# Optimization experiments

Hardware: AMD Instinct MI355X
Metric: run time of the kernel (lower is better)

Reference implementation:

```python
import jax, jax.numpy as jnp
import numpy as np

B, N, F_IN, F_OUT = 8, 8192, 128, 128
E = 1_048_576
BN = B * N


def setup_inputs() -> dict:
    key = jax.random.key(0)
    ks = jax.random.split(key, 9)
    glorot = (6.0 / (F_IN + F_OUT)) ** 0.5
    return {
        "X": jax.random.normal(ks[0], (B, N, F_IN), dtype=jnp.float32),
        "W0": jax.random.uniform(ks[1], (F_IN, F_OUT), jnp.float32, -glorot, glorot),
        "W1": jax.random.uniform(ks[2], (F_IN, F_OUT), jnp.float32, -glorot, glorot),
        "rows0": jax.random.randint(ks[3], (E,), 0, BN, dtype=jnp.int32),
        "cols0": jax.random.randint(ks[4], (E,), 0, BN, dtype=jnp.int32),
        "vals0": jax.random.uniform(ks[5], (E,), dtype=jnp.float32),
        "rows1": jax.random.randint(ks[6], (E,), 0, BN, dtype=jnp.int32),
        "cols1": jax.random.randint(ks[7], (E,), 0, BN, dtype=jnp.int32),
        "vals1": jax.random.uniform(ks[8], (E,), dtype=jnp.float32),
    }


def _spmm(rows, cols, vals, H, n):
    # COO sparse [n, n] @ dense H [n, F]: gather source rows, scale, scatter-add.
    return jax.ops.segment_sum(vals[:, None] * H[cols], rows, num_segments=n)


def reference(X, W0, W1, rows0, cols0, vals0, rows1, cols1, vals1):
    b, n, f_in = X.shape
    X2 = X.reshape(-1, f_in)                      # [B*N, F_in]
    h0 = _spmm(rows0, cols0, vals0, X2 @ W0, b * n)  # filter_0 @ (X W0)
    h1 = _spmm(rows1, cols1, vals1, X2 @ W1, b * n)  # filter_1 @ (X W1)
    out = jax.nn.relu(h0 + h1).reshape(b, n, -1)  # add_n + relu
    return out
```

## Files before the change

kernel.cpp:

```cpp
#include <hip/hip_runtime.h>


typedef unsigned int   uint;
typedef unsigned short ushort;
typedef unsigned char  uchar;
typedef float f32x4 __attribute__((ext_vector_type(4)));
typedef int   i32x4 __attribute__((ext_vector_type(4)));

constexpr int NB  = 256;
constexpr int EPB = 8192;

__device__ __forceinline__ ushort f2bf(float f) {
    uint u = __float_as_uint(f);
    u += 0x7fffu + ((u >> 16) & 1u);
    return (ushort)(u >> 16);
}
__device__ __forceinline__ float bf2f(ushort h) {
    return __uint_as_float((uint)h << 16);
}

#define ACC_FENCE(a) asm volatile("s_nop 7\n\ts_nop 7" : "+v"(a))

__global__ __launch_bounds__(64) void w_swz(const float* __restrict__ W0,
                                            const float* __restrict__ W1,
                                            uint4* __restrict__ Wswz) {
    const int bx = blockIdx.x;
    const int f  = bx >> 5;
    const int ct = (bx >> 2) & 7;
    const int kt = bx & 3;
    const int l  = threadIdx.x;
    const float* W = f ? W1 : W0;
    const int kbase = kt * 32 + (l >> 4) * 8;
    const int col   = ct * 16 + (l & 15);
    ushort h[8];
#pragma unroll
    for (int j = 0; j < 8; ++j)
        h[j] = f2bf(W[(kbase + j) * 128 + col]);
    uint4 o;
    o.x = (uint)h[0] | ((uint)h[1] << 16);
    o.y = (uint)h[2] | ((uint)h[3] << 16);
    o.z = (uint)h[4] | ((uint)h[5] << 16);
    o.w = (uint)h[6] | ((uint)h[7] << 16);
    Wswz[((f * 8 + ct) * 4 + kt) * 64 + l] = o;
}

__global__ __launch_bounds__(256) void gemm_mfma(const float* __restrict__ X,
                                                 const i32x4* __restrict__ Wswz,
                                                 ushort* __restrict__ H, int BN) {
    __shared__ ushort xs_hi[64][136];
    __shared__ ushort xs_lo[64][136];
    const int tid = threadIdx.x;
    const int l = tid & 63;
    const int w = tid >> 6;
    const long rbase = (long)blockIdx.x * 64;

    const float4* Xv = reinterpret_cast<const float4*>(X + rbase * 128);
#pragma unroll
    for (int i = 0; i < 8; ++i) {
        int idx = i * 256 + tid;
        int row = idx >> 5, c4 = idx & 31;
        float4 v = Xv[idx];
        ushort4 hi, lo;
        hi.x = f2bf(v.x); lo.x = f2bf(v.x - bf2f(hi.x));
        hi.y = f2bf(v.y); lo.y = f2bf(v.y - bf2f(hi.y));
        hi.z = f2bf(v.z); lo.z = f2bf(v.z - bf2f(hi.z));
        hi.w = f2bf(v.w); lo.w = f2bf(v.w - bf2f(hi.w));
        *reinterpret_cast<ushort4*>(&xs_hi[row][c4 * 4]) = hi;
        *reinterpret_cast<ushort4*>(&xs_lo[row][c4 * 4]) = lo;
    }
    __syncthreads();

    i32x4 a_hi[4], a_lo[4];
    const int arow = w * 16 + (l & 15);
    const int kb = (l >> 4) * 8;
#pragma unroll
    for (int kt = 0; kt < 4; ++kt) {
        a_hi[kt] = *reinterpret_cast<const i32x4*>(&xs_hi[arow][kt * 32 + kb]);
        a_lo[kt] = *reinterpret_cast<const i32x4*>(&xs_lo[arow][kt * 32 + kb]);
    }

    f32x4 acc[2][8];
#pragma unroll
    for (int f = 0; f < 2; ++f)
#pragma unroll
        for (int ct = 0; ct < 8; ++ct)
            acc[f][ct] = (f32x4)0.0f;

#pragma unroll
    for (int ct = 0; ct < 8; ++ct)
#pragma unroll
        for (int f = 0; f < 2; ++f)
#pragma unroll
            for (int kt = 0; kt < 4; ++kt) {
                i32x4 b = Wswz[((f * 8 + ct) * 4 + kt) * 64 + l];
                asm volatile("v_mfma_f32_16x16x32_bf16 %0, %1, %2, %0"
                             : "+v"(acc[f][ct]) : "v"(a_hi[kt]), "v"(b));
                asm volatile("v_mfma_f32_16x16x32_bf16 %0, %1, %2, %0"
                             : "+v"(acc[f][ct]) : "v"(a_lo[kt]), "v"(b));
            }

#pragma unroll
    for (int ct = 0; ct < 8; ++ct)
#pragma unroll
        for (int f = 0; f < 2; ++f) {
            f32x4 a = acc[f][ct];
            ACC_FENCE(a);
            ushort* Hf = H + (size_t)f * BN * 128;
            size_t base = (size_t)(rbase + w * 16 + (l >> 4) * 4) * 128
                        + ct * 16 + (l & 15);
            Hf[base]       = f2bf(a.x);
            Hf[base + 128] = f2bf(a.y);
            Hf[base + 256] = f2bf(a.z);
            Hf[base + 384] = f2bf(a.w);
        }
}

__global__ __launch_bounds__(256) void hist_coarse(const int* __restrict__ r0,
                                                   const int* __restrict__ r1,
                                                   int* __restrict__ cnt, int E) {
    __shared__ int h[NB];
    const int f = blockIdx.y, t = threadIdx.x;
    const int* rows = f ? r1 : r0;
    h[t] = 0;
    __syncthreads();
    const int base = blockIdx.x * EPB;
    for (int k = 0; k < EPB / 256; ++k) {
        int e = base + k * 256 + t;
        if (e < E) atomicAdd(&h[rows[e] >> 8], 1);
    }
    __syncthreads();
    if (h[t]) atomicAdd(&cnt[f * NB + t], h[t]);
}

__global__ __launch_bounds__(256) void scan_coarse(const int* __restrict__ cnt,
                                                   int* __restrict__ bbase,
                                                   int* __restrict__ bcur,
                                                   int* __restrict__ row_ptr,
                                                   int rp_stride, int BN, int E) {
    __shared__ int s[NB];
    const int f = blockIdx.x, t = threadIdx.x;
    int v = cnt[f * NB + t];
    s[t] = v;
    __syncthreads();
    for (int off = 1; off < NB; off <<= 1) {
        int u = (t >= off) ? s[t - off] : 0;
        __syncthreads();
        s[t] += u;
        __syncthreads();
    }
    int base = s[t] - v;
    bbase[f * NB + t] = base;
    bcur [f * NB + t] = base;
    if (t == NB - 1) row_ptr[(size_t)f * rp_stride + BN] = E;
}

__global__ __launch_bounds__(256) void partition(const int* __restrict__ r0,
                                                 const int* __restrict__ c0,
                                                 const float* __restrict__ v0,
                                                 const int* __restrict__ r1,
                                                 const int* __restrict__ c1,
                                                 const float* __restrict__ v1,
                                                 int* __restrict__ bcur,
                                                 uint* __restrict__ cvy,
                                                 uchar* __restrict__ cvr, int E) {
    __shared__ int h[NB];
    __shared__ int cur[NB];
    const int f = blockIdx.y, t = threadIdx.x;
    const int*   rows = f ? r1 : r0;
    const int*   cols = f ? c1 : c0;
    const float* vals = f ? v1 : v0;
    const int base = blockIdx.x * EPB;

    h[t] = 0;
    __syncthreads();
    for (int k = 0; k < EPB / 256; ++k) {
        int e = base + k * 256 + t;
        if (e < E) atomicAdd(&h[rows[e] >> 8], 1);
    }
    __syncthreads();
    cur[t] = atomicAdd(&bcur[f * NB + t], h[t]);
    __syncthreads();

    uint*  yout = cvy + (size_t)f * E;
    uchar* rout = cvr + (size_t)f * E;
    for (int k = 0; k < EPB / 256; ++k) {
        int e = base + k * 256 + t;
        if (e < E) {
            int r = rows[e];
            int pos = atomicAdd(&cur[r >> 8], 1);
            yout[pos] = ((uint)cols[e] << 16) | (uint)f2bf(vals[e]);
            rout[pos] = (uchar)(r & 255);
        }
    }
}

__global__ __launch_bounds__(256) void bucket_sort(const uint* __restrict__ cvy,
                                                   const uchar* __restrict__ cvr,
                                                   const int* __restrict__ bbase,
                                                   const int* __restrict__ bcur,
                                                   uint* __restrict__ cv,
                                                   int* __restrict__ row_ptr,
                                                   int rp_stride, int E) {
    __shared__ int h[NB];
    __shared__ int s[NB];
    __shared__ int curs[NB];
    const int f = blockIdx.y, b = blockIdx.x, t = threadIdx.x;
    const int start = bbase[f * NB + b];
    const int end   = bcur [f * NB + b];
    const uint*  yin = cvy + (size_t)f * E;
    const uchar* rin = cvr + (size_t)f * E;

    h[t] = 0;
    __syncthreads();
    for (int i = start + t; i < end; i += 256)
        atomicAdd(&h[rin[i]], 1);
    __syncthreads();

    int v = h[t];
    s[t] = v;
    __syncthreads();
    for (int off = 1; off < NB; off <<= 1) {
        int u = (t >= off) ? s[t - off] : 0;
        __syncthreads();
        s[t] += u;
        __syncthreads();
    }
    int rowbase = start + s[t] - v;
    row_ptr[(size_t)f * rp_stride + b * 256 + t] = rowbase;
    curs[t] = rowbase;
    __syncthreads();

    uint* outp = cv + (size_t)f * E;
    for (int i = start + t; i < end; i += 256) {
        int pos = atomicAdd(&curs[rin[i]], 1);
        outp[pos] = yin[i];
    }
}

__global__ __launch_bounds__(256) void hist2(const int* __restrict__ r0,
                                             const int* __restrict__ r1,
                                             int* __restrict__ cnt, int E, int BN) {
    int e = blockIdx.x * 256 + threadIdx.x;
    const int* rows = blockIdx.y ? r1 : r0;
    if (e < E) atomicAdd(&cnt[(size_t)blockIdx.y * BN + rows[e]], 1);
}

__global__ __launch_bounds__(256) void scan2(int* __restrict__ cnt,
                                             int* __restrict__ row_ptr,
                                             int n, int rp_stride) {
    __shared__ int ssum[256];
    int* counts = cnt + (size_t)blockIdx.x * n;
    int* rp     = row_ptr + (size_t)blockIdx.x * rp_stride;
    const int t = threadIdx.x;
    const int chunk = n / 256;
    const int base = t * chunk;
    const int4* c4 = reinterpret_cast<const int4*>(counts + base);
    int s = 0;
#pragma unroll 4
    for (int i = 0; i < chunk / 4; ++i) {
        int4 v = c4[i];
        s += v.x + v.y + v.z + v.w;
    }
    ssum[t] = s;
    __syncthreads();
    for (int off = 1; off < 256; off <<= 1) {
        int u = (t >= off) ? ssum[t - off] : 0;
        __syncthreads();
        ssum[t] += u;
        __syncthreads();
    }
    int run = ssum[t] - s;
    int4* rp4 = reinterpret_cast<int4*>(rp + base);
    int4* cu4 = reinterpret_cast<int4*>(counts + base);
#pragma unroll 4
    for (int i = 0; i < chunk / 4; ++i) {
        int4 v = c4[i];
        int4 p;
        p.x = run; run += v.x;
        p.y = run; run += v.y;
        p.z = run; run += v.z;
        p.w = run; run += v.w;
        rp4[i] = p;
        cu4[i] = p;
    }
    if (t == 255) rp[n] = run;
}

__global__ __launch_bounds__(256) void permute2(const int* __restrict__ r0,
                                                const int* __restrict__ c0,
                                                const float* __restrict__ v0,
                                                const int* __restrict__ r1,
                                                const int* __restrict__ c1,
                                                const float* __restrict__ v1,
                                                int* __restrict__ cursor,
                                                uint* __restrict__ cv, int E, int BN) {
    int f = blockIdx.y;
    const int*   rows = f ? r1 : r0;
    const int*   cols = f ? c1 : c0;
    const float* vals = f ? v1 : v0;
    int e = blockIdx.x * 256 + threadIdx.x;
    if (e < E) {
        int r = rows[e];
        int pos = atomicAdd(&cursor[(size_t)f * BN + r], 1);
        cv[(size_t)f * E + pos] = ((uint)cols[e] << 16) | (uint)f2bf(vals[e]);
    }
}

__device__ __forceinline__ void fma4(float4& a, float v, ushort4 h) {
    a.x = fmaf(v, bf2f(h.x), a.x);
    a.y = fmaf(v, bf2f(h.y), a.y);
    a.z = fmaf(v, bf2f(h.z), a.z);
    a.w = fmaf(v, bf2f(h.w), a.w);
}

__global__ __launch_bounds__(256) void gather_fused(const int* __restrict__ row_ptr,
                                                    int rp_stride,
                                                    const uint* __restrict__ cv, int E,
                                                    const ushort* __restrict__ H, int BN,
                                                    float* __restrict__ out) {
    const int half = threadIdx.x >> 5;
    const int sub  = threadIdx.x & 31;
    const int r = blockIdx.x * 8 + half;

    float4 a0 = make_float4(0.f, 0.f, 0.f, 0.f);
    float4 a1 = make_float4(0.f, 0.f, 0.f, 0.f);
    float4 a2 = make_float4(0.f, 0.f, 0.f, 0.f);
    float4 a3 = make_float4(0.f, 0.f, 0.f, 0.f);

#pragma unroll
    for (int f = 0; f < 2; ++f) {
        const int*    rp  = row_ptr + (size_t)f * rp_stride;
        const uint*   cvf = cv + (size_t)f * E;
        const ushort* Hf  = H + (size_t)f * BN * 128;
        int e = rp[r];
        const int t = rp[r + 1];
        for (; e + 7 < t; e += 8) {
            uint p0 = cvf[e],     p1 = cvf[e + 1], p2 = cvf[e + 2], p3 = cvf[e + 3];
            uint p4 = cvf[e + 4], p5 = cvf[e + 5], p6 = cvf[e + 6], p7 = cvf[e + 7];
            ushort4 h0 = reinterpret_cast<const ushort4*>(Hf + (size_t)(p0 >> 16) * 128)[sub];
            ushort4 h1 = reinterpret_cast<const ushort4*>(Hf + (size_t)(p1 >> 16) * 128)[sub];
            ushort4 h2 = reinterpret_cast<const ushort4*>(Hf + (size_t)(p2 >> 16) * 128)[sub];
            ushort4 h3 = reinterpret_cast<const ushort4*>(Hf + (size_t)(p3 >> 16) * 128)[sub];
            ushort4 h4 = reinterpret_cast<const ushort4*>(Hf + (size_t)(p4 >> 16) * 128)[sub];
            ushort4 h5 = reinterpret_cast<const ushort4*>(Hf + (size_t)(p5 >> 16) * 128)[sub];
            ushort4 h6 = reinterpret_cast<const ushort4*>(Hf + (size_t)(p6 >> 16) * 128)[sub];
            ushort4 h7 = reinterpret_cast<const ushort4*>(Hf + (size_t)(p7 >> 16) * 128)[sub];
            fma4(a0, __uint_as_float(p0 << 16), h0);
            fma4(a1, __uint_as_float(p1 << 16), h1);
            fma4(a2, __uint_as_float(p2 << 16), h2);
            fma4(a3, __uint_as_float(p3 << 16), h3);
            fma4(a0, __uint_as_float(p4 << 16), h4);
            fma4(a1, __uint_as_float(p5 << 16), h5);
            fma4(a2, __uint_as_float(p6 << 16), h6);
            fma4(a3, __uint_as_float(p7 << 16), h7);
        }
        for (; e + 3 < t; e += 4) {
            uint p0 = cvf[e], p1 = cvf[e + 1], p2 = cvf[e + 2], p3 = cvf[e + 3];
            ushort4 h0 = reinterpret_cast<const ushort4*>(Hf + (size_t)(p0 >> 16) * 128)[sub];
            ushort4 h1 = reinterpret_cast<const ushort4*>(Hf + (size_t)(p1 >> 16) * 128)[sub];
            ushort4 h2 = reinterpret_cast<const ushort4*>(Hf + (size_t)(p2 >> 16) * 128)[sub];
            ushort4 h3 = reinterpret_cast<const ushort4*>(Hf + (size_t)(p3 >> 16) * 128)[sub];
            fma4(a0, __uint_as_float(p0 << 16), h0);
            fma4(a1, __uint_as_float(p1 << 16), h1);
            fma4(a2, __uint_as_float(p2 << 16), h2);
            fma4(a3, __uint_as_float(p3 << 16), h3);
        }
        for (; e < t; ++e) {
            uint p0 = cvf[e];
            ushort4 h0 = reinterpret_cast<const ushort4*>(Hf + (size_t)(p0 >> 16) * 128)[sub];
            fma4(a0, __uint_as_float(p0 << 16), h0);
        }
    }

    float4 o;
    o.x = fmaxf((a0.x + a1.x) + (a2.x + a3.x), 0.0f);
    o.y = fmaxf((a0.y + a1.y) + (a2.y + a3.y), 0.0f);
    o.z = fmaxf((a0.z + a1.z) + (a2.z + a3.z), 0.0f);
    o.w = fmaxf((a0.w + a1.w) + (a2.w + a3.w), 0.0f);
    reinterpret_cast<float4*>(out)[(size_t)r * 32 + sub] = o;
}

extern "C" void kernel_launch(void* const* d_in, const int* in_sizes, int n_in,
                              void* d_out, int out_size, void* d_ws, size_t ws_size,
                              hipStream_t stream) {
    const float* X     = (const float*)d_in[0];
    const float* W0    = (const float*)d_in[1];
    const float* W1    = (const float*)d_in[2];
    const int*   rows0 = (const int*)d_in[3];
    const int*   cols0 = (const int*)d_in[4];
    const float* vals0 = (const float*)d_in[5];
    const int*   rows1 = (const int*)d_in[6];
    const int*   cols1 = (const int*)d_in[7];
    const float* vals1 = (const float*)d_in[8];
    float* out = (float*)d_out;

    const int BN = in_sizes[0] / 128;
    const int E  = in_sizes[3];
    const int rp_stride = BN + 16;

    char* ws = (char*)d_ws;
    size_t off = 0;
    auto alloc = [&](size_t bytes) {
        void* p = ws + off;
        off = (off + bytes + 255) & ~(size_t)255;
        return p;
    };
    ushort* H       = (ushort*)alloc((size_t)2 * BN * 128 * sizeof(ushort));
    uint*   cv      = (uint*)  alloc((size_t)2 * E * sizeof(uint));
    int*    row_ptr = (int*)   alloc((size_t)2 * rp_stride * sizeof(int));
    uint4*  Wswz    = (uint4*) alloc((size_t)2 * 128 * 128 * sizeof(ushort));

    const size_t need_big = off + (size_t)2 * E * sizeof(uint)
                                + (size_t)2 * E * sizeof(uchar)
                                + 3 * (size_t)2 * NB * sizeof(int) + 1024;

    const int gath_blocks = BN / 8;

    w_swz<<<64, 64, 0, stream>>>(W0, W1, Wswz);
    gemm_mfma<<<BN / 64, 256, 0, stream>>>(X, (const i32x4*)Wswz, H, BN);

    if (ws_size >= need_big && BN == 65536) {
        uint*  cvy   = (uint*) alloc((size_t)2 * E * sizeof(uint));
        uchar* cvr   = (uchar*)alloc((size_t)2 * E * sizeof(uchar));
        int*   cnt   = (int*)  alloc((size_t)2 * NB * sizeof(int));
        int*   bbase = (int*)  alloc((size_t)2 * NB * sizeof(int));
        int*   bcur  = (int*)  alloc((size_t)2 * NB * sizeof(int));

        const int part_blocks = (E + EPB - 1) / EPB;
        hipMemsetAsync(cnt, 0, (size_t)2 * NB * sizeof(int), stream);
        hist_coarse<<<dim3(part_blocks, 2), 256, 0, stream>>>(rows0, rows1, cnt, E);
        scan_coarse<<<2, 256, 0, stream>>>(cnt, bbase, bcur, row_ptr, rp_stride, BN, E);
        partition<<<dim3(part_blocks, 2), 256, 0, stream>>>(rows0, cols0, vals0,
                                                            rows1, cols1, vals1,
                                                            bcur, cvy, cvr, E);
        bucket_sort<<<dim3(NB, 2), 256, 0, stream>>>(cvy, cvr, bbase, bcur,
                                                     cv, row_ptr, rp_stride, E);
    } else {
        int* cursor = (int*)alloc((size_t)2 * BN * sizeof(int));
        const int edge_blocks = (E + 255) / 256;
        hipMemsetAsync(cursor, 0, (size_t)2 * BN * sizeof(int), stream);
        hist2<<<dim3(edge_blocks, 2), 256, 0, stream>>>(rows0, rows1, cursor, E, BN);
        scan2<<<2, 256, 0, stream>>>(cursor, row_ptr, BN, rp_stride);
        permute2<<<dim3(edge_blocks, 2), 256, 0, stream>>>(rows0, cols0, vals0,
                                                           rows1, cols1, vals1,
                                                           cursor, cv, E, BN);
    }

    gather_fused<<<gath_blocks, 256, 0, stream>>>(row_ptr, rp_stride, cv, E, H, BN, out);
}
```

Before: 179.1 us.

## Fuse column-bucket partition with GEMM and make row sort stable by column

```diff
diff --git a/kernel.cpp b/kernel.cpp
--- a/kernel.cpp
+++ b/kernel.cpp
@@ -44,15 +44,113 @@
     Wswz[((f * 8 + ct) * 4 + kt) * 64 + l] = o;
 }
 
-__global__ __launch_bounds__(256) void gemm_mfma(const float* __restrict__ X,
-                                                 const i32x4* __restrict__ Wswz,
-                                                 ushort* __restrict__ H, int BN) {
+__global__ __launch_bounds__(256) void hist_both(const int* __restrict__ r0,
+                                                 const int* __restrict__ c0,
+                                                 const int* __restrict__ r1,
+                                                 const int* __restrict__ c1,
+                                                 int* __restrict__ cnt_col,
+                                                 int* __restrict__ cnt_row, int E) {
+    __shared__ int hc[NB], hr[NB];
+    const int f = blockIdx.y, t = threadIdx.x;
+    const int* rows = f ? r1 : r0;
+    const int* cols = f ? c1 : c0;
+    hc[t] = 0; hr[t] = 0;
+    __syncthreads();
+    const int base = blockIdx.x * EPB;
+    for (int k = 0; k < EPB / 256; ++k) {
+        int e = base + k * 256 + t;
+        if (e < E) {
+            atomicAdd(&hc[cols[e] >> 8], 1);
+            atomicAdd(&hr[rows[e] >> 8], 1);
+        }
+    }
+    __syncthreads();
+    if (hc[t]) atomicAdd(&cnt_col[f * NB + t], hc[t]);
+    if (hr[t]) atomicAdd(&cnt_row[f * NB + t], hr[t]);
+}
+
+__global__ __launch_bounds__(256) void scan_both(const int* __restrict__ cnt_col,
+                                                 const int* __restrict__ cnt_row,
+                                                 int* __restrict__ ccur,
+                                                 int* __restrict__ bbase,
+                                                 int* __restrict__ bcur,
+                                                 int* __restrict__ row_ptr,
+                                                 int rp_stride, int BN, int E) {
+    __shared__ int s[NB];
+    const int bx = blockIdx.x, t = threadIdx.x;
+    const int kind = bx >> 1, f = bx & 1;
+    const int* cnt = kind ? cnt_row : cnt_col;
+    int v = cnt[f * NB + t];
+    s[t] = v;
+    __syncthreads();
+    for (int off = 1; off < NB; off <<= 1) {
+        int u = (t >= off) ? s[t - off] : 0;
+        __syncthreads();
+        s[t] += u;
+        __syncthreads();
+    }
+    int base = s[t] - v;
+    if (kind == 0) {
+        ccur[f * NB + t] = base;
+    } else {
+        bbase[f * NB + t] = base;
+        bcur [f * NB + t] = base;
+        if (t == NB - 1) row_ptr[(size_t)f * rp_stride + BN] = E;
+    }
+}
+
+__global__ __launch_bounds__(256) void fused_p0_gemm(
+        const float* __restrict__ X, const i32x4* __restrict__ Wswz,
+        ushort* __restrict__ H, int BN,
+        const int* __restrict__ r0, const int* __restrict__ c0,
+        const float* __restrict__ v0,
+        const int* __restrict__ r1, const int* __restrict__ c1,
+        const float* __restrict__ v1,
+        int* __restrict__ ccur, uint* __restrict__ colv,
+        ushort* __restrict__ crow, int E, int partb) {
     __shared__ ushort xs_hi[64][136];
     __shared__ ushort xs_lo[64][136];
+    __shared__ int ph[NB], pcur[NB];
+
+    const int bx  = blockIdx.x;
     const int tid = threadIdx.x;
+
+    if (bx < 2 * partb) {
+        const int f  = bx / partb;
+        const int px = bx % partb;
+        const int*   rows = f ? r1 : r0;
+        const int*   cols = f ? c1 : c0;
+        const float* vals = f ? v1 : v0;
+        const int base = px * EPB;
+
+        ph[tid] = 0;
+        __syncthreads();
+        for (int k = 0; k < EPB / 256; ++k) {
+            int e = base + k * 256 + tid;
+            if (e < E) atomicAdd(&ph[cols[e] >> 8], 1);
+        }
+        __syncthreads();
+        pcur[tid] = atomicAdd(&ccur[f * NB + tid], ph[tid]);
+        __syncthreads();
+
+        uint*   yo = colv + (size_t)f * E;
+        ushort* ro = crow + (size_t)f * E;
+        for (int k = 0; k < EPB / 256; ++k) {
+            int e = base + k * 256 + tid;
+            if (e < E) {
+                int c = cols[e];
+                int pos = atomicAdd(&pcur[c >> 8], 1);
+                yo[pos] = ((uint)c << 16) | (uint)f2bf(vals[e]);
+                ro[pos] = (ushort)rows[e];
+            }
+        }
+        return;
+    }
+
+    const int gx = bx - 2 * partb;
     const int l = tid & 63;
     const int w = tid >> 6;
-    const long rbase = (long)blockIdx.x * 64;
+    const long rbase = (long)gx * 64;
 
     const float4* Xv = reinterpret_cast<const float4*>(X + rbase * 128);
 #pragma unroll
@@ -113,6 +211,83 @@
             Hf[base + 256] = f2bf(a.z);
             Hf[base + 384] = f2bf(a.w);
         }
+}
+
+__global__ __launch_bounds__(256) void partition_row2(const uint* __restrict__ colv,
+                                                      const ushort* __restrict__ crow,
+                                                      int* __restrict__ bcur,
+                                                      uint* __restrict__ cvy,
+                                                      uchar* __restrict__ cvr, int E) {
+    __shared__ int h[NB], cur[NB];
+    const int f = blockIdx.y, t = threadIdx.x;
+    const uint*   cvl = colv + (size_t)f * E;
+    const ushort* cr  = crow + (size_t)f * E;
+    const int base = blockIdx.x * EPB;
+
+    h[t] = 0;
+    __syncthreads();
+    for (int k = 0; k < EPB / 256; ++k) {
+        int e = base + k * 256 + t;
+        if (e < E) atomicAdd(&h[cr[e] >> 8], 1);
+    }
+    __syncthreads();
+    cur[t] = atomicAdd(&bcur[f * NB + t], h[t]);
+    __syncthreads();
+
+    uint*  yo = cvy + (size_t)f * E;
+    uchar* ro = cvr + (size_t)f * E;
+    for (int k = 0; k < EPB / 256; ++k) {
+        int e = base + k * 256 + t;
+        if (e < E) {
+            ushort r = cr[e];
+            int pos = atomicAdd(&cur[r >> 8], 1);
+            yo[pos] = cvl[e];
+            ro[pos] = (uchar)(r & 255);
+        }
+    }
+}
+
+__global__ __launch_bounds__(256) void bucket_sort(const uint* __restrict__ cvy,
+                                                   const uchar* __restrict__ cvr,
+                                                   const int* __restrict__ bbase,
+                                                   const int* __restrict__ bcur,
+                                                   uint* __restrict__ cv,
+                                                   int* __restrict__ row_ptr,
+                                                   int rp_stride, int E) {
+    __shared__ int h[NB];
+    __shared__ int s[NB];
+    __shared__ int curs[NB];
+    const int f = blockIdx.y, b = blockIdx.x, t = threadIdx.x;
+    const int start = bbase[f * NB + b];
+    const int end   = bcur [f * NB + b];
+    const uint*  yin = cvy + (size_t)f * E;
+    const uchar* rin = cvr + (size_t)f * E;
+
+    h[t] = 0;
+    __syncthreads();
+    for (int i = start + t; i < end; i += 256)
+        atomicAdd(&h[rin[i]], 1);
+    __syncthreads();
+
+    int v = h[t];
+    s[t] = v;
+    __syncthreads();
+    for (int off = 1; off < NB; off <<= 1) {
+        int u = (t >= off) ? s[t - off] : 0;
+        __syncthreads();
+        s[t] += u;
+        __syncthreads();
+    }
+    int rowbase = start + s[t] - v;
+    row_ptr[(size_t)f * rp_stride + b * 256 + t] = rowbase;
+    curs[t] = rowbase;
+    __syncthreads();
+
+    uint* outp = cv + (size_t)f * E;
+    for (int i = start + t; i < end; i += 256) {
+        int pos = atomicAdd(&curs[rin[i]], 1);
+        outp[pos] = yin[i];
+    }
 }
 
 __global__ __launch_bounds__(256) void hist_coarse(const int* __restrict__ r0,
@@ -194,47 +369,75 @@
     }
 }
 
-__global__ __launch_bounds__(256) void bucket_sort(const uint* __restrict__ cvy,
-                                                   const uchar* __restrict__ cvr,
-                                                   const int* __restrict__ bbase,
-                                                   const int* __restrict__ bcur,
-                                                   uint* __restrict__ cv,
-                                                   int* __restrict__ row_ptr,
-                                                   int rp_stride, int E) {
-    __shared__ int h[NB];
-    __shared__ int s[NB];
-    __shared__ int curs[NB];
-    const int f = blockIdx.y, b = blockIdx.x, t = threadIdx.x;
-    const int start = bbase[f * NB + b];
-    const int end   = bcur [f * NB + b];
-    const uint*  yin = cvy + (size_t)f * E;
-    const uchar* rin = cvr + (size_t)f * E;
-
-    h[t] = 0;
-    __syncthreads();
-    for (int i = start + t; i < end; i += 256)
-        atomicAdd(&h[rin[i]], 1);
-    __syncthreads();
-
-    int v = h[t];
-    s[t] = v;
-    __syncthreads();
-    for (int off = 1; off < NB; off <<= 1) {
-        int u = (t >= off) ? s[t - off] : 0;
-        __syncthreads();
-        s[t] += u;
-        __syncthreads();
-    }
-    int rowbase = start + s[t] - v;
-    row_ptr[(size_t)f * rp_stride + b * 256 + t] = rowbase;
-    curs[t] = rowbase;
-    __syncthreads();
-
-    uint* outp = cv + (size_t)f * E;
-    for (int i = start + t; i < end; i += 256) {
-        int pos = atomicAdd(&curs[rin[i]], 1);
-        outp[pos] = yin[i];
-    }
+__global__ __launch_bounds__(256) void gemm_mfma(const float* __restrict__ X,
+                                                 const i32x4* __restrict__ Wswz,
+                                                 ushort* __restrict__ H, int BN) {
+    __shared__ ushort xs_hi[64][136];
+    __shared__ ushort xs_lo[64][136];
+    const int tid = threadIdx.x;
+    const int l = tid & 63;
+    const int w = tid >> 6;
+    const long rbase = (long)blockIdx.x * 64;
+
+    const float4* Xv = reinterpret_cast<const float4*>(X + rbase * 128);
+#pragma unroll
+    for (int i = 0; i < 8; ++i) {
+        int idx = i * 256 + tid;
+        int row = idx >> 5, c4 = idx & 31;
+        float4 v = Xv[idx];
+        ushort4 hi, lo;
+        hi.x = f2bf(v.x); lo.x = f2bf(v.x - bf2f(hi.x));
+        hi.y = f2bf(v.y); lo.y = f2bf(v.y - bf2f(hi.y));
+        hi.z = f2bf(v.z); lo.z = f2bf(v.z - bf2f(hi.z));
+        hi.w = f2bf(v.w); lo.w = f2bf(v.w - bf2f(hi.w));
+        *reinterpret_cast<ushort4*>(&xs_hi[row][c4 * 4]) = hi;
+        *reinterpret_cast<ushort4*>(&xs_lo[row][c4 * 4]) = lo;
+    }
+    __syncthreads();
+
+    i32x4 a_hi[4], a_lo[4];
+    const int arow = w * 16 + (l & 15);
+    const int kb = (l >> 4) * 8;
+#pragma unroll
+    for (int kt = 0; kt < 4; ++kt) {
+        a_hi[kt] = *reinterpret_cast<const i32x4*>(&xs_hi[arow][kt * 32 + kb]);
+        a_lo[kt] = *reinterpret_cast<const i32x4*>(&xs_lo[arow][kt * 32 + kb]);
+    }
+
+    f32x4 acc[2][8];
+#pragma unroll
+    for (int f = 0; f < 2; ++f)
+#pragma unroll
+        for (int ct = 0; ct < 8; ++ct)
+            acc[f][ct] = (f32x4)0.0f;
+
+#pragma unroll
+    for (int ct = 0; ct < 8; ++ct)
+#pragma unroll
+        for (int f = 0; f < 2; ++f)
+#pragma unroll
+            for (int kt = 0; kt < 4; ++kt) {
+                i32x4 b = Wswz[((f * 8 + ct) * 4 + kt) * 64 + l];
+                asm volatile("v_mfma_f32_16x16x32_bf16 %0, %1, %2, %0"
+                             : "+v"(acc[f][ct]) : "v"(a_hi[kt]), "v"(b));
+                asm volatile("v_mfma_f32_16x16x32_bf16 %0, %1, %2, %0"
+                             : "+v"(acc[f][ct]) : "v"(a_lo[kt]), "v"(b));
+            }
+
+#pragma unroll
+    for (int ct = 0; ct < 8; ++ct)
+#pragma unroll
+        for (int f = 0; f < 2; ++f) {
+            f32x4 a = acc[f][ct];
+            ACC_FENCE(a);
+            ushort* Hf = H + (size_t)f * BN * 128;
+            size_t base = (size_t)(rbase + w * 16 + (l >> 4) * 4) * 128
+                        + ct * 16 + (l & 15);
+            Hf[base]       = f2bf(a.x);
+            Hf[base + 128] = f2bf(a.y);
+            Hf[base + 256] = f2bf(a.z);
+            Hf[base + 384] = f2bf(a.w);
+        }
 }
 
 __global__ __launch_bounds__(256) void hist2(const int* __restrict__ r0,
@@ -397,6 +600,8 @@
     const int BN = in_sizes[0] / 128;
     const int E  = in_sizes[3];
     const int rp_stride = BN + 16;
+    const int partb = (E + EPB - 1) / EPB;
+    const int gath_blocks = BN / 8;
 
     char* ws = (char*)d_ws;
     size_t off = 0;
@@ -406,34 +611,66 @@
         return p;
     };
     ushort* H       = (ushort*)alloc((size_t)2 * BN * 128 * sizeof(ushort));
-    uint*   cv      = (uint*)  alloc((size_t)2 * E * sizeof(uint));
     int*    row_ptr = (int*)   alloc((size_t)2 * rp_stride * sizeof(int));
     uint4*  Wswz    = (uint4*) alloc((size_t)2 * 128 * 128 * sizeof(ushort));
-
-    const size_t need_big = off + (size_t)2 * E * sizeof(uint)
-                                + (size_t)2 * E * sizeof(uchar)
-                                + 3 * (size_t)2 * NB * sizeof(int) + 1024;
-
-    const int gath_blocks = BN / 8;
+    const size_t common = off;
+
+    uint*   colv = (uint*)  alloc((size_t)2 * E * sizeof(uint));
+    ushort* crow = (ushort*)alloc((size_t)2 * E * sizeof(ushort));
+    uint*   cvy  = (uint*)  alloc((size_t)2 * E * sizeof(uint));
+    uchar*  cvr  = (uchar*) alloc((size_t)2 * E * sizeof(uchar));
+    int*    cnts = (int*)   alloc((size_t)4 * NB * sizeof(int));
+    int*    ccur = (int*)   alloc((size_t)2 * NB * sizeof(int));
+    int*    bbase= (int*)   alloc((size_t)2 * NB * sizeof(int));
+    int*    bcur = (int*)   alloc((size_t)2 * NB * sizeof(int));
+    const size_t need_new = off;
+    uint* cv_new = colv;
 
     w_swz<<<64, 64, 0, stream>>>(W0, W1, Wswz);
+
+    if (ws_size >= need_new && BN == 65536) {
+        int* cnt_col = cnts;
+        int* cnt_row = cnts + 2 * NB;
+        hipMemsetAsync(cnts, 0, (size_t)4 * NB * sizeof(int), stream);
+        hist_both<<<dim3(partb, 2), 256, 0, stream>>>(rows0, cols0, rows1, cols1,
+                                                      cnt_col, cnt_row, E);
+        scan_both<<<4, 256, 0, stream>>>(cnt_col, cnt_row, ccur, bbase, bcur,
+                                         row_ptr, rp_stride, BN, E);
+        fused_p0_gemm<<<2 * partb + BN / 64, 256, 0, stream>>>(
+            X, (const i32x4*)Wswz, H, BN,
+            rows0, cols0, vals0, rows1, cols1, vals1,
+            ccur, colv, crow, E, partb);
+        partition_row2<<<dim3(partb, 2), 256, 0, stream>>>(colv, crow, bcur,
+                                                           cvy, cvr, E);
+        bucket_sort<<<dim3(NB, 2), 256, 0, stream>>>(cvy, cvr, bbase, bcur,
+                                                     cv_new, row_ptr, rp_stride, E);
+        gather_fused<<<gath_blocks, 256, 0, stream>>>(row_ptr, rp_stride, cv_new,
+                                                      E, H, BN, out);
+        return;
+    }
+
+    off = common;
+    uint* cv = (uint*)alloc((size_t)2 * E * sizeof(uint));
+    const size_t need_r7 = off + (size_t)2 * E * sizeof(uint)
+                               + (size_t)2 * E * sizeof(uchar)
+                               + 3 * (size_t)2 * NB * sizeof(int) + 1024;
+
     gemm_mfma<<<BN / 64, 256, 0, stream>>>(X, (const i32x4*)Wswz, H, BN);
 
-    if (ws_size >= need_big && BN == 65536) {
-        uint*  cvy   = (uint*) alloc((size_t)2 * E * sizeof(uint));
-        uchar* cvr   = (uchar*)alloc((size_t)2 * E * sizeof(uchar));
+    if (ws_size >= need_r7 && BN == 65536) {
+        uint*  cvy2  = (uint*) alloc((size_t)2 * E * sizeof(uint));
+        uchar* cvr2  = (uchar*)alloc((size_t)2 * E * sizeof(uchar));
         int*   cnt   = (int*)  alloc((size_t)2 * NB * sizeof(int));
-        int*   bbase = (int*)  alloc((size_t)2 * NB * sizeof(int));
-        int*   bcur  = (int*)  alloc((size_t)2 * NB * sizeof(int));
-
-        const int part_blocks = (E + EPB - 1) / EPB;
+        int*   bb2   = (int*)  alloc((size_t)2 * NB * sizeof(int));
+        int*   bc2   = (int*)  alloc((size_t)2 * NB * sizeof(int));
+
         hipMemsetAsync(cnt, 0, (size_t)2 * NB * sizeof(int), stream);
-        hist_coarse<<<dim3(part_blocks, 2), 256, 0, stream>>>(rows0, rows1, cnt, E);
-        scan_coarse<<<2, 256, 0, stream>>>(cnt, bbase, bcur, row_ptr, rp_stride, BN, E);
-        partition<<<dim3(part_blocks, 2), 256, 0, stream>>>(rows0, cols0, vals0,
-                                                            rows1, cols1, vals1,
-                                                            bcur, cvy, cvr, E);
-        bucket_sort<<<dim3(NB, 2), 256, 0, stream>>>(cvy, cvr, bbase, bcur,
+        hist_coarse<<<dim3(partb, 2), 256, 0, stream>>>(rows0, rows1, cnt, E);
+        scan_coarse<<<2, 256, 0, stream>>>(cnt, bb2, bc2, row_ptr, rp_stride, BN, E);
+        partition<<<dim3(partb, 2), 256, 0, stream>>>(rows0, cols0, vals0,
+                                                      rows1, cols1, vals1,
+                                                      bc2, cvy2, cvr2, E);
+        bucket_sort<<<dim3(NB, 2), 256, 0, stream>>>(cvy2, cvr2, bb2, bc2,
                                                      cv, row_ptr, rp_stride, E);
     } else {
         int* cursor = (int*)alloc((size_t)2 * BN * sizeof(int));
```

Measured after the change: 218.6 us. +22.0%, slower.

## Fuse per-bucket row sort into the SpMM gather kernel using LDS

Applied to the files above, without the earlier changes.

```diff
diff --git a/kernel.cpp b/kernel.cpp
--- a/kernel.cpp
+++ b/kernel.cpp
@@ -9,6 +9,7 @@
 
 constexpr int NB  = 256;
 constexpr int EPB = 8192;
+constexpr int CAP = 8192;
 
 __device__ __forceinline__ ushort f2bf(float f) {
     uint u = __float_as_uint(f);
@@ -134,9 +135,7 @@
 
 __global__ __launch_bounds__(256) void scan_coarse(const int* __restrict__ cnt,
                                                    int* __restrict__ bbase,
-                                                   int* __restrict__ bcur,
-                                                   int* __restrict__ row_ptr,
-                                                   int rp_stride, int BN, int E) {
+                                                   int* __restrict__ bcur) {
     __shared__ int s[NB];
     const int f = blockIdx.x, t = threadIdx.x;
     int v = cnt[f * NB + t];
@@ -151,7 +150,6 @@
     int base = s[t] - v;
     bbase[f * NB + t] = base;
     bcur [f * NB + t] = base;
-    if (t == NB - 1) row_ptr[(size_t)f * rp_stride + BN] = E;
 }
 
 __global__ __launch_bounds__(256) void partition(const int* __restrict__ r0,
@@ -194,118 +192,6 @@
     }
 }
 
-__global__ __launch_bounds__(256) void bucket_sort(const uint* __restrict__ cvy,
-                                                   const uchar* __restrict__ cvr,
-                                                   const int* __restrict__ bbase,
-                                                   const int* __restrict__ bcur,
-                                                   uint* __restrict__ cv,
-                                                   int* __restrict__ row_ptr,
-                                                   int rp_stride, int E) {
-    __shared__ int h[NB];
-    __shared__ int s[NB];
-    __shared__ int curs[NB];
-    const int f = blockIdx.y, b = blockIdx.x, t = threadIdx.x;
-    const int start = bbase[f * NB + b];
-    const int end   = bcur [f * NB + b];
-    const uint*  yin = cvy + (size_t)f * E;
-    const uchar* rin = cvr + (size_t)f * E;
-
-    h[t] = 0;
-    __syncthreads();
-    for (int i = start + t; i < end; i += 256)
-        atomicAdd(&h[rin[i]], 1);
-    __syncthreads();
-
-    int v = h[t];
-    s[t] = v;
-    __syncthreads();
-    for (int off = 1; off < NB; off <<= 1) {
-        int u = (t >= off) ? s[t - off] : 0;
-        __syncthreads();
-        s[t] += u;
-        __syncthreads();
-    }
-    int rowbase = start + s[t] - v;
-    row_ptr[(size_t)f * rp_stride + b * 256 + t] = rowbase;
-    curs[t] = rowbase;
-    __syncthreads();
-
-    uint* outp = cv + (size_t)f * E;
-    for (int i = start + t; i < end; i += 256) {
-        int pos = atomicAdd(&curs[rin[i]], 1);
-        outp[pos] = yin[i];
-    }
-}
-
-__global__ __launch_bounds__(256) void hist2(const int* __restrict__ r0,
-                                             const int* __restrict__ r1,
-                                             int* __restrict__ cnt, int E, int BN) {
-    int e = blockIdx.x * 256 + threadIdx.x;
-    const int* rows = blockIdx.y ? r1 : r0;
-    if (e < E) atomicAdd(&cnt[(size_t)blockIdx.y * BN + rows[e]], 1);
-}
-
-__global__ __launch_bounds__(256) void scan2(int* __restrict__ cnt,
-                                             int* __restrict__ row_ptr,
-                                             int n, int rp_stride) {
-    __shared__ int ssum[256];
-    int* counts = cnt + (size_t)blockIdx.x * n;
-    int* rp     = row_ptr + (size_t)blockIdx.x * rp_stride;
-    const int t = threadIdx.x;
-    const int chunk = n / 256;
-    const int base = t * chunk;
-    const int4* c4 = reinterpret_cast<const int4*>(counts + base);
-    int s = 0;
-#pragma unroll 4
-    for (int i = 0; i < chunk / 4; ++i) {
-        int4 v = c4[i];
-        s += v.x + v.y + v.z + v.w;
-    }
-    ssum[t] = s;
-    __syncthreads();
-    for (int off = 1; off < 256; off <<= 1) {
-        int u = (t >= off) ? ssum[t - off] : 0;
-        __syncthreads();
-        ssum[t] += u;
-        __syncthreads();
-    }
-    int run = ssum[t] - s;
-    int4* rp4 = reinterpret_cast<int4*>(rp + base);
-    int4* cu4 = reinterpret_cast<int4*>(counts + base);
-#pragma unroll 4
-    for (int i = 0; i < chunk / 4; ++i) {
-        int4 v = c4[i];
-        int4 p;
-        p.x = run; run += v.x;
-        p.y = run; run += v.y;
-        p.z = run; run += v.z;
-        p.w = run; run += v.w;
-        rp4[i] = p;
-        cu4[i] = p;
-    }
-    if (t == 255) rp[n] = run;
-}
-
-__global__ __launch_bounds__(256) void permute2(const int* __restrict__ r0,
-                                                const int* __restrict__ c0,
-                                                const float* __restrict__ v0,
-                                                const int* __restrict__ r1,
-                                                const int* __restrict__ c1,
-                                                const float* __restrict__ v1,
-                                                int* __restrict__ cursor,
-                                                uint* __restrict__ cv, int E, int BN) {
-    int f = blockIdx.y;
-    const int*   rows = f ? r1 : r0;
-    const int*   cols = f ? c1 : c0;
-    const float* vals = f ? v1 : v0;
-    int e = blockIdx.x * 256 + threadIdx.x;
-    if (e < E) {
-        int r = rows[e];
-        int pos = atomicAdd(&cursor[(size_t)f * BN + r], 1);
-        cv[(size_t)f * E + pos] = ((uint)cols[e] << 16) | (uint)f2bf(vals[e]);
-    }
-}
-
 __device__ __forceinline__ void fma4(float4& a, float v, ushort4 h) {
     a.x = fmaf(v, bf2f(h.x), a.x);
     a.y = fmaf(v, bf2f(h.y), a.y);
@@ -313,71 +199,144 @@
     a.w = fmaf(v, bf2f(h.w), a.w);
 }
 
-__global__ __launch_bounds__(256) void gather_fused(const int* __restrict__ row_ptr,
-                                                    int rp_stride,
-                                                    const uint* __restrict__ cv, int E,
-                                                    const ushort* __restrict__ H, int BN,
-                                                    float* __restrict__ out) {
-    const int half = threadIdx.x >> 5;
-    const int sub  = threadIdx.x & 31;
-    const int r = blockIdx.x * 8 + half;
-
-    float4 a0 = make_float4(0.f, 0.f, 0.f, 0.f);
-    float4 a1 = make_float4(0.f, 0.f, 0.f, 0.f);
-    float4 a2 = make_float4(0.f, 0.f, 0.f, 0.f);
-    float4 a3 = make_float4(0.f, 0.f, 0.f, 0.f);
-
-#pragma unroll
+__global__ __launch_bounds__(1024) void sort_gather(
+        const uint* __restrict__ cvy, const uchar* __restrict__ cvr,
+        const int* __restrict__ bbase, const int* __restrict__ bcur,
+        const ushort* __restrict__ H, int BN,
+        float* __restrict__ out, int E) {
+    __shared__ uint cvl[2][CAP];
+    __shared__ int rp[2][NB + 1];
+    __shared__ int hcnt[NB];
+    __shared__ int curs[NB];
+    __shared__ int sstart[2], scount[2], sovf[2];
+
+    const int b = blockIdx.x;
+    const int t = threadIdx.x;
+
+#pragma unroll 1
     for (int f = 0; f < 2; ++f) {
-        const int*    rp  = row_ptr + (size_t)f * rp_stride;
-        const uint*   cvf = cv + (size_t)f * E;
-        const ushort* Hf  = H + (size_t)f * BN * 128;
-        int e = rp[r];
-        const int t = rp[r + 1];
-        for (; e + 7 < t; e += 8) {
-            uint p0 = cvf[e],     p1 = cvf[e + 1], p2 = cvf[e + 2], p3 = cvf[e + 3];
-            uint p4 = cvf[e + 4], p5 = cvf[e + 5], p6 = cvf[e + 6], p7 = cvf[e + 7];
-            ushort4 h0 = reinterpret_cast<const ushort4*>(Hf + (size_t)(p0 >> 16) * 128)[sub];
-            ushort4 h1 = reinterpret_cast<const ushort4*>(Hf + (size_t)(p1 >> 16) * 128)[sub];
-            ushort4 h2 = reinterpret_cast<const ushort4*>(Hf + (size_t)(p2 >> 16) * 128)[sub];
-            ushort4 h3 = reinterpret_cast<const ushort4*>(Hf + (size_t)(p3 >> 16) * 128)[sub];
-            ushort4 h4 = reinterpret_cast<const ushort4*>(Hf + (size_t)(p4 >> 16) * 128)[sub];
-            ushort4 h5 = reinterpret_cast<const ushort4*>(Hf + (size_t)(p5 >> 16) * 128)[sub];
-            ushort4 h6 = reinterpret_cast<const ushort4*>(Hf + (size_t)(p6 >> 16) * 128)[sub];
-            ushort4 h7 = reinterpret_cast<const ushort4*>(Hf + (size_t)(p7 >> 16) * 128)[sub];
-            fma4(a0, __uint_as_float(p0 << 16), h0);
-            fma4(a1, __uint_as_float(p1 << 16), h1);
-            fma4(a2, __uint_as_float(p2 << 16), h2);
-            fma4(a3, __uint_as_float(p3 << 16), h3);
-            fma4(a0, __uint_as_float(p4 << 16), h4);
-            fma4(a1, __uint_as_float(p5 << 16), h5);
-            fma4(a2, __uint_as_float(p6 << 16), h6);
-            fma4(a3, __uint_as_float(p7 << 16), h7);
-        }
-        for (; e + 3 < t; e += 4) {
-            uint p0 = cvf[e], p1 = cvf[e + 1], p2 = cvf[e + 2], p3 = cvf[e + 3];
-            ushort4 h0 = reinterpret_cast<const ushort4*>(Hf + (size_t)(p0 >> 16) * 128)[sub];
-            ushort4 h1 = reinterpret_cast<const ushort4*>(Hf + (size_t)(p1 >> 16) * 128)[sub];
-            ushort4 h2 = reinterpret_cast<const ushort4*>(Hf + (size_t)(p2 >> 16) * 128)[sub];
-            ushort4 h3 = reinterpret_cast<const ushort4*>(Hf + (size_t)(p3 >> 16) * 128)[sub];
-            fma4(a0, __uint_as_float(p0 << 16), h0);
-            fma4(a1, __uint_as_float(p1 << 16), h1);
-            fma4(a2, __uint_as_float(p2 << 16), h2);
-            fma4(a3, __uint_as_float(p3 << 16), h3);
-        }
-        for (; e < t; ++e) {
-            uint p0 = cvf[e];
-            ushort4 h0 = reinterpret_cast<const ushort4*>(Hf + (size_t)(p0 >> 16) * 128)[sub];
-            fma4(a0, __uint_as_float(p0 << 16), h0);
-        }
-    }
-
-    float4 o;
-    o.x = fmaxf((a0.x + a1.x) + (a2.x + a3.x), 0.0f);
-    o.y = fmaxf((a0.y + a1.y) + (a2.y + a3.y), 0.0f);
-    o.z = fmaxf((a0.z + a1.z) + (a2.z + a3.z), 0.0f);
-    o.w = fmaxf((a0.w + a1.w) + (a2.w + a3.w), 0.0f);
-    reinterpret_cast<float4*>(out)[(size_t)r * 32 + sub] = o;
+        if (t == 0) {
+            int s0 = bbase[f * NB + b];
+            int e0 = bcur [f * NB + b];
+            sstart[f] = s0;
+            scount[f] = e0 - s0;
+            sovf[f]   = (e0 - s0) > CAP;
+        }
+        if (t < NB) hcnt[t] = 0;
+        __syncthreads();
+        const int s = sstart[f], n = scount[f];
+        const uchar* rin = cvr + (size_t)f * E + s;
+        const uint*  yin = cvy + (size_t)f * E + s;
+        for (int i = t; i < n; i += 1024)
+            atomicAdd(&hcnt[rin[i]], 1);
+        __syncthreads();
+        int v = (t < NB) ? hcnt[t] : 0;
+        if (t < NB) curs[t] = v;
+        __syncthreads();
+        for (int off = 1; off < NB; off <<= 1) {
+            int u = 0;
+            if (t < NB && t >= off) u = curs[t - off];
+            __syncthreads();
+            if (t < NB) curs[t] += u;
+            __syncthreads();
+        }
+        if (t < NB) {
+            int ex = curs[t] - v;
+            rp[f][t] = ex;
+            curs[t] = ex;
+        }
+        if (t == 0) rp[f][NB] = n;
+        __syncthreads();
+        if (!sovf[f]) {
+            for (int i = t; i < n; i += 1024) {
+                uchar r = rin[i];
+                int pos = atomicAdd(&curs[r], 1);
+                cvl[f][pos] = __builtin_nontemporal_load(&yin[i]);
+            }
+        }
+        __syncthreads();
+    }
+
+    const int half = t >> 5;
+    const int sub  = t & 31;
+    f32x4* outv = reinterpret_cast<f32x4*>(out);
+
+#pragma unroll 1
+    for (int k = 0; k < 8; ++k) {
+        const int lr = k * 32 + half;
+        const long gr = (long)b * NB + lr;
+
+        float4 a0 = make_float4(0.f, 0.f, 0.f, 0.f);
+        float4 a1 = make_float4(0.f, 0.f, 0.f, 0.f);
+        float4 a2 = make_float4(0.f, 0.f, 0.f, 0.f);
+        float4 a3 = make_float4(0.f, 0.f, 0.f, 0.f);
+
+#pragma unroll
+        for (int f = 0; f < 2; ++f) {
+            const ushort* Hf = H + (size_t)f * BN * 128;
+            if (!sovf[f]) {
+                int e = rp[f][lr];
+                const int e1 = rp[f][lr + 1];
+                for (; e + 7 < e1; e += 8) {
+                    uint p0 = cvl[f][e],     p1 = cvl[f][e + 1];
+                    uint p2 = cvl[f][e + 2], p3 = cvl[f][e + 3];
+                    uint p4 = cvl[f][e + 4], p5 = cvl[f][e + 5];
+                    uint p6 = cvl[f][e + 6], p7 = cvl[f][e + 7];
+                    ushort4 h0 = reinterpret_cast<const ushort4*>(Hf + (size_t)(p0 >> 16) * 128)[sub];
+                    ushort4 h1 = reinterpret_cast<const ushort4*>(Hf + (size_t)(p1 >> 16) * 128)[sub];
+                    ushort4 h2 = reinterpret_cast<const ushort4*>(Hf + (size_t)(p2 >> 16) * 128)[sub];
+                    ushort4 h3 = reinterpret_cast<const ushort4*>(Hf + (size_t)(p3 >> 16) * 128)[sub];
+                    ushort4 h4 = reinterpret_cast<const ushort4*>(Hf + (size_t)(p4 >> 16) * 128)[sub];
+                    ushort4 h5 = reinterpret_cast<const ushort4*>(Hf + (size_t)(p5 >> 16) * 128)[sub];
+                    ushort4 h6 = reinterpret_cast<const ushort4*>(Hf + (size_t)(p6 >> 16) * 128)[sub];
+                    ushort4 h7 = reinterpret_cast<const ushort4*>(Hf + (size_t)(p7 >> 16) * 128)[sub];
+                    fma4(a0, __uint_as_float(p0 << 16), h0);
+                    fma4(a1, __uint_as_float(p1 << 16), h1);
+                    fma4(a2, __uint_as_float(p2 << 16), h2);
+                    fma4(a3, __uint_as_float(p3 << 16), h3);
+                    fma4(a0, __uint_as_float(p4 << 16), h4);
+                    fma4(a1, __uint_as_float(p5 << 16), h5);
+                    fma4(a2, __uint_as_float(p6 << 16), h6);
+                    fma4(a3, __uint_as_float(p7 << 16), h7);
+                }
+                for (; e + 3 < e1; e += 4) {
+                    uint p0 = cvl[f][e],     p1 = cvl[f][e + 1];
+                    uint p2 = cvl[f][e + 2], p3 = cvl[f][e + 3];
+                    ushort4 h0 = reinterpret_cast<const ushort4*>(Hf + (size_t)(p0 >> 16) * 128)[sub];
+                    ushort4 h1 = reinterpret_cast<const ushort4*>(Hf + (size_t)(p1 >> 16) * 128)[sub];
+                    ushort4 h2 = reinterpret_cast<const ushort4*>(Hf + (size_t)(p2 >> 16) * 128)[sub];
+                    ushort4 h3 = reinterpret_cast<const ushort4*>(Hf + (size_t)(p3 >> 16) * 128)[sub];
+                    fma4(a0, __uint_as_float(p0 << 16), h0);
+                    fma4(a1, __uint_as_float(p1 << 16), h1);
+                    fma4(a2, __uint_as_float(p2 << 16), h2);
+                    fma4(a3, __uint_as_float(p3 << 16), h3);
+                }
+                for (; e < e1; ++e) {
+                    uint p0 = cvl[f][e];
+                    ushort4 h0 = reinterpret_cast<const ushort4*>(Hf + (size_t)(p0 >> 16) * 128)[sub];
+                    fma4(a0, __uint_as_float(p0 << 16), h0);
+                }
+            } else {
+                const int s = sstart[f], n = scount[f];
+                const uchar* rin = cvr + (size_t)f * E + s;
+                const uint*  yin = cvy + (size_t)f * E + s;
+                for (int i = 0; i < n; ++i) {
+                    if (rin[i] == (uchar)lr) {
+                        uint p0 = yin[i];
+                        ushort4 h0 = reinterpret_cast<const ushort4*>(Hf + (size_t)(p0 >> 16) * 128)[sub];
+                        fma4(a0, __uint_as_float(p0 << 16), h0);
+                    }
+                }
+            }
+        }
+
+        f32x4 o;
+        o.x = fmaxf((a0.x + a1.x) + (a2.x + a3.x), 0.0f);
+        o.y = fmaxf((a0.y + a1.y) + (a2.y + a3.y), 0.0f);
+        o.z = fmaxf((a0.z + a1.z) + (a2.z + a3.z), 0.0f);
+        o.w = fmaxf((a0.w + a1.w) + (a2.w + a3.w), 0.0f);
+        __builtin_nontemporal_store(o, outv + gr * 32 + sub);
+    }
 }
 
 extern "C" void kernel_launch(void* const* d_in, const int* in_sizes, int n_in,
@@ -396,7 +355,7 @@
 
     const int BN = in_sizes[0] / 128;
     const int E  = in_sizes[3];
-    const int rp_stride = BN + 16;
+    const int partb = (E + EPB - 1) / EPB;
 
     char* ws = (char*)d_ws;
     size_t off = 0;
@@ -405,46 +364,22 @@
         off = (off + bytes + 255) & ~(size_t)255;
         return p;
     };
-    ushort* H       = (ushort*)alloc((size_t)2 * BN * 128 * sizeof(ushort));
-    uint*   cv      = (uint*)  alloc((size_t)2 * E * sizeof(uint));
-    int*    row_ptr = (int*)   alloc((size_t)2 * rp_stride * sizeof(int));
-    uint4*  Wswz    = (uint4*) alloc((size_t)2 * 128 * 128 * sizeof(ushort));
-
-    const size_t need_big = off + (size_t)2 * E * sizeof(uint)
-                                + (size_t)2 * E * sizeof(uchar)
-                                + 3 * (size_t)2 * NB * sizeof(int) + 1024;
-
-    const int gath_blocks = BN / 8;
+    ushort* H     = (ushort*)alloc((size_t)2 * BN * 128 * sizeof(ushort));
+    uint4*  Wswz  = (uint4*) alloc((size_t)2 * 128 * 128 * sizeof(ushort));
+    uint*   cvy   = (uint*)  alloc((size_t)2 * E * sizeof(uint));
+    uchar*  cvr   = (uchar*) alloc((size_t)2 * E * sizeof(uchar));
+    int*    cnt   = (int*)   alloc((size_t)2 * NB * sizeof(int));
+    int*    bbase = (int*)   alloc((size_t)2 * NB * sizeof(int));
+    int*    bcur  = (int*)   alloc((size_t)2 * NB * sizeof(int));
 
     w_swz<<<64, 64, 0, stream>>>(W0, W1, Wswz);
     gemm_mfma<<<BN / 64, 256, 0, stream>>>(X, (const i32x4*)Wswz, H, BN);
 
-    if (ws_size >= need_big && BN == 65536) {
-        uint*  cvy   = (uint*) alloc((size_t)2 * E * sizeof(uint));
-        uchar* cvr   = (uchar*)alloc((size_t)2 * E * sizeof(uchar));
-        int*   cnt   = (int*)  alloc((size_t)2 * NB * sizeof(int));
-        int*   bbase = (int*)  alloc((size_t)2 * NB * sizeof(int));
-        int*   bcur  = (int*)  alloc((size_t)2 * NB * sizeof(int));
-
-        const int part_blocks = (E + EPB - 1) / EPB;
-        hipMemsetAsync(cnt, 0, (size_t)2 * NB * sizeof(int), stream);
-        hist_coarse<<<dim3(part_blocks, 2), 256, 0, stream>>>(rows0, rows1, cnt, E);
-        scan_coarse<<<2, 256, 0, stream>>>(cnt, bbase, bcur, row_ptr, rp_stride, BN, E);
-        partition<<<dim3(part_blocks, 2), 256, 0, stream>>>(rows0, cols0, vals0,
-                                                            rows1, cols1, vals1,
-                                                            bcur, cvy, cvr, E);
-        bucket_sort<<<dim3(NB, 2), 256, 0, stream>>>(cvy, cvr, bbase, bcur,
-                                                     cv, row_ptr, rp_stride, E);
-    } else {
-        int* cursor = (int*)alloc((size_t)2 * BN * sizeof(int));
-        const int edge_blocks = (E + 255) / 256;
-        hipMemsetAsync(cursor, 0, (size_t)2 * BN * sizeof(int), stream);
-        hist2<<<dim3(edge_blocks, 2), 256, 0, stream>>>(rows0, rows1, cursor, E, BN);
-        scan2<<<2, 256, 0, stream>>>(cursor, row_ptr, BN, rp_stride);
-        permute2<<<dim3(edge_blocks, 2), 256, 0, stream>>>(rows0, cols0, vals0,
-                                                           rows1, cols1, vals1,
-                                                           cursor, cv, E, BN);
-    }
-
-    gather_fused<<<gath_blocks, 256, 0, stream>>>(row_ptr, rp_stride, cv, E, H, BN, out);
-}
+    hipMemsetAsync(cnt, 0, (size_t)2 * NB * sizeof(int), stream);
+    hist_coarse<<<dim3(partb, 2), 256, 0, stream>>>(rows0, rows1, cnt, E);
+    scan_coarse<<<2, 256, 0, stream>>>(cnt, bbase, bcur);
+    partition<<<dim3(partb, 2), 256, 0, stream>>>(rows0, cols0, vals0,
+                                                  rows1, cols1, vals1,
+                                                  bcur, cvy, cvr, E);
+    sort_gather<<<NB, 1024, 0, stream>>>(cvy, cvr, bbase, bcur, H, BN, out, E);
+}
```

Result: faster. 166.9 us (-6.8%).
